# Optimization experiments

Hardware: AMD Instinct MI355X
Metric: run time of the kernel (lower is better)

The kernel has to match this reference:

```python
import jax, jax.numpy as jnp
import numpy as np
import math

N = 50000        # nodes
E = 800000       # edges (avg degree 16)
F_IN = 128
F_OUT = 64


def setup_inputs() -> dict:
    key = jax.random.key(0)
    k = jax.random.split(key, 7)
    stdv = 1.0 / math.sqrt(F_OUT)
    x = jax.random.normal(k[0], (N, F_IN), dtype=jnp.float32)
    t = jax.random.uniform(k[1], (N,), dtype=jnp.float32)
    src = jax.random.randint(k[2], (E,), 0, N, dtype=jnp.int64)
    dst = jax.random.randint(k[3], (E,), 0, N, dtype=jnp.int64)
    # sparse adjacency values (e.g. normalized adjacency weights)
    edge_vals = jax.random.uniform(k[4], (E,), dtype=jnp.float32)
    weight = jax.random.uniform(k[5], (F_IN, F_OUT), dtype=jnp.float32,
                                minval=-stdv, maxval=stdv)
    bias = jax.random.uniform(k[6], (F_OUT,), dtype=jnp.float32,
                              minval=-stdv, maxval=stdv)
    return {"x": x, "t": t, "src": src, "dst": dst,
            "edge_vals": edge_vals, "weight": weight, "bias": bias}


def reference(x, t, src, dst, edge_vals, weight, bias):
    # support = (X @ W) * t[:, None]   -- dense GEMM + per-row scale
    support = (x @ weight) * t[:, None]                 # [N, F_OUT]
    # spmm(adj, support): gather rows at src, scale by edge value, reduce by dst
    msgs = support[src] * edge_vals[:, None]            # [E, F_OUT]
    out = jax.ops.segment_sum(msgs, dst, num_segments=N)  # [N, F_OUT]
    return out + bias
```

## Files before the change

kernel.cpp:

```cpp
#include <hip/hip_runtime.h>
#include <hip/hip_bf16.h>

#define FIN 128
#define FOUT 64
#define TILE_ROWS 64

#define EPB 2048
#define NPB 32
#define NBUK_MAX 1600
#define CAP 768

#define OFF_HIST      6400000
#define OFF_BLOCKSUMS 8860000
#define OFF_TMP       8861024

#define SCAN_CHUNK 4096

typedef short bf16x8 __attribute__((ext_vector_type(8)));
typedef float f32x4  __attribute__((ext_vector_type(4)));

__device__ inline ushort f32_to_bf16_rne(float f) {
    unsigned u = __float_as_uint(f);
    u += 0x7FFFu + ((u >> 16) & 1u);
    return (ushort)(u >> 16);
}
__device__ inline float bf16_to_f32(ushort h) {
    return __uint_as_float((unsigned)h << 16);
}

union __align__(16) GemmHistSh {
    int    h[NBUK_MAX];
    ushort wt[FOUT * FIN];
};

__global__ __launch_bounds__(256) void gemm_hist_kernel(
    const float* __restrict__ x, const float* __restrict__ t,
    const float* __restrict__ W, ushort* __restrict__ support, int N,
    const int* __restrict__ dst, int* __restrict__ hist,
    int E, int SBP, int NBUK, int G, int GB)
{
    __shared__ GemmHistSh sh;
    const int tid = threadIdx.x;

    if (blockIdx.x >= GB) {
        const int hb    = blockIdx.x - GB;
        const int chunk = (hb & 7) * G + (hb >> 3);
        for (int i = tid; i < NBUK; i += 256) sh.h[i] = 0;
        __syncthreads();
        const int e0 = chunk * EPB;
        for (int i = tid; i < EPB; i += 256) {
            int e = e0 + i;
            if (e < E) atomicAdd(&sh.h[dst[e] >> 5], 1);
        }
        __syncthreads();
        for (int i = tid; i < NBUK; i += 256)
            hist[i * SBP + chunk] = sh.h[i];
        return;
    }

    const int lane = tid & 63;
    const int w    = tid >> 6;
    const int ln   = lane & 15;
    const int q    = lane >> 4;
    const int rowb = blockIdx.x * TILE_ROWS + w * 16;
    const int arow = rowb + ln;

    for (int idx = tid; idx < FIN * FOUT; idx += 256) {
        int k = idx >> 6;
        int n = idx & 63;
        sh.wt[n * FIN + (k ^ ((n & 7) << 3))] = f32_to_bf16_rne(W[idx]);
    }
    __syncthreads();

    f32x4 acc[4];
    #pragma unroll
    for (int nt = 0; nt < 4; ++nt)
        #pragma unroll
        for (int r = 0; r < 4; ++r) acc[nt][r] = 0.f;

    const bool aok = (arow < N);
    const float* xrow = &x[(size_t)arow * FIN];

    #pragma unroll
    for (int kc = 0; kc < 4; ++kc) {
        float xs[8];
        #pragma unroll
        for (int j = 0; j < 8; ++j) xs[j] = 0.f;
        if (aok) {
            float4 x0 = *(const float4*)&xrow[kc * 32 + q * 8];
            float4 x1 = *(const float4*)&xrow[kc * 32 + q * 8 + 4];
            xs[0] = x0.x; xs[1] = x0.y; xs[2] = x0.z; xs[3] = x0.w;
            xs[4] = x1.x; xs[5] = x1.y; xs[6] = x1.z; xs[7] = x1.w;
        }
        bf16x8 a;
        #pragma unroll
        for (int j = 0; j < 8; ++j) a[j] = (short)f32_to_bf16_rne(xs[j]);

        const int k0 = kc * 32 + q * 8;
        #pragma unroll
        for (int nt = 0; nt < 4; ++nt) {
            bf16x8 b = *(const bf16x8*)
                &sh.wt[(nt * 16 + ln) * FIN + (k0 ^ ((ln & 7) << 3))];
            acc[nt] = __builtin_amdgcn_mfma_f32_16x16x32_bf16(a, b, acc[nt], 0, 0, 0);
        }
    }

    #pragma unroll
    for (int reg = 0; reg < 4; ++reg) {
        int r = rowb + q * 4 + reg;
        if (r < N) {
            float tv = t[r];
            #pragma unroll
            for (int nt = 0; nt < 4; ++nt)
                support[(size_t)r * FOUT + nt * 16 + ln] =
                    f32_to_bf16_rne(acc[nt][reg] * tv);
        }
    }
}

__global__ __launch_bounds__(256) void scan_sums_kernel(
    const int* __restrict__ counts, int* __restrict__ blocksums, int M)
{
    __shared__ int red[256];
    const int tid  = threadIdx.x;
    const int base = blockIdx.x * SCAN_CHUNK + tid * 16;

    int s = 0;
    #pragma unroll
    for (int v = 0; v < 4; ++v) {
        int idx = base + v * 4;
        if (idx + 3 < M) {
            int4 c = *(const int4*)&counts[idx];
            s += c.x + c.y + c.z + c.w;
        } else {
            for (int i = 0; i < 4; ++i)
                if (idx + i < M) s += counts[idx + i];
        }
    }
    red[tid] = s;
    __syncthreads();
    #pragma unroll
    for (int d = 128; d > 0; d >>= 1) {
        if (tid < d) red[tid] += red[tid + d];
        __syncthreads();
    }
    if (tid == 0) blocksums[blockIdx.x] = red[0];
}

__global__ __launch_bounds__(256) void scan_apply_kernel(
    int* __restrict__ counts, const int* __restrict__ blocksums, int M, int NB)
{
    __shared__ int s[256];
    __shared__ int bex;
    const int tid  = threadIdx.x;
    const int base = blockIdx.x * SCAN_CHUNK + tid * 16;

    if (tid < 64) {
        int carry = 0;
        for (int w0 = 0; w0 < NB; w0 += 64) {
            int idx = w0 + tid;
            int v   = (idx < NB) ? blocksums[idx] : 0;
            int val = v;
            #pragma unroll
            for (int d = 1; d < 64; d <<= 1) {
                int n = __shfl_up(val, d);
                if (tid >= d) val += n;
            }
            if (idx == (int)blockIdx.x) bex = carry + val - v;
            carry += __shfl(val, 63);
        }
    }

    int c[16];
    int mysum = 0;
    #pragma unroll
    for (int v = 0; v < 4; ++v) {
        int idx = base + v * 4;
        int4 cc = make_int4(0, 0, 0, 0);
        if (idx + 3 < M) {
            cc = *(const int4*)&counts[idx];
        } else {
            if (idx + 0 < M) cc.x = counts[idx + 0];
            if (idx + 1 < M) cc.y = counts[idx + 1];
            if (idx + 2 < M) cc.z = counts[idx + 2];
            if (idx + 3 < M) cc.w = counts[idx + 3];
        }
        c[v * 4 + 0] = cc.x; c[v * 4 + 1] = cc.y;
        c[v * 4 + 2] = cc.z; c[v * 4 + 3] = cc.w;
        mysum += cc.x + cc.y + cc.z + cc.w;
    }
    s[tid] = mysum;
    __syncthreads();
    #pragma unroll
    for (int d = 1; d < 256; d <<= 1) {
        int add = (tid >= d) ? s[tid - d] : 0;
        __syncthreads();
        s[tid] += add;
        __syncthreads();
    }
    int ex = bex + s[tid] - mysum;
    #pragma unroll
    for (int i = 0; i < 16; ++i) {
        if (base + i < M) {
            counts[base + i] = ex;
            ex += c[i];
        }
    }
}

__global__ __launch_bounds__(256) void coarse_scatter_kernel(
    const int* __restrict__ src, const int* __restrict__ dst,
    const float* __restrict__ ev, const int* __restrict__ scanned,
    int2* __restrict__ tmp, int E, int SBP, int NBUK, int G)
{
    __shared__ int cur[NBUK_MAX];
    const int tid   = threadIdx.x;
    const int b     = blockIdx.x;
    const int chunk = (b & 7) * G + (b >> 3);
    for (int i = tid; i < NBUK; i += 256)
        cur[i] = scanned[i * SBP + chunk];
    __syncthreads();

    const int e0 = chunk * EPB;
    for (int i = tid; i < EPB; i += 256) {
        int e = e0 + i;
        if (e < E) {
            int d   = dst[e];
            int pos = atomicAdd(&cur[d >> 5], 1);
            tmp[pos] = make_int2(src[e] | ((d & (NPB - 1)) << 16),
                                 __float_as_int(ev[e]));
        }
    }
}

__global__ __launch_bounds__(256) void bucket_gather_kernel(
    const int* __restrict__ scanned, const int2* __restrict__ tmp,
    const ushort* __restrict__ support, const float* __restrict__ bias,
    float* __restrict__ out, int E, int N, int SBP, int NBUK)
{
    __shared__ int2 raw[CAP];
    __shared__ int2 sorted[CAP];
    __shared__ int  cnt[NPB];
    __shared__ int  starts[NPB + 1];
    __shared__ int  cur[NPB];

    const int tid   = threadIdx.x;
    const int w     = tid >> 6;
    const int lane  = tid & 63;
    const int B     = blockIdx.x;
    const int node0 = B * NPB;

    const int base   = scanned[B * SBP];
    const int endB   = (B + 1 < NBUK) ? scanned[(B + 1) * SBP] : E;
    const int nrec   = endB - base;
    const int placed = (nrec < CAP) ? nrec : CAP;

    if (tid < NPB) cnt[tid] = 0;
    __syncthreads();

    for (int i = tid; i < placed; i += 256) {
        int2 r = tmp[base + i];
        raw[i] = r;
        atomicAdd(&cnt[(r.x >> 16) & (NPB - 1)], 1);
    }
    __syncthreads();

    if (tid < 64) {
        int v   = (tid < NPB) ? cnt[tid] : 0;
        int val = v;
        #pragma unroll
        for (int d = 1; d < NPB; d <<= 1) {
            int n = __shfl_up(val, d);
            if (tid >= d) val += n;
        }
        if (tid < NPB) {
            starts[tid] = val - v;
            cur[tid]    = val - v;
        }
        if (tid == 0) starts[NPB] = placed;
    }
    __syncthreads();

    for (int i = tid; i < placed; i += 256) {
        int2 r  = raw[i];
        int pos = atomicAdd(&cur[(r.x >> 16) & (NPB - 1)], 1);
        sorted[pos] = r;
    }
    __syncthreads();

    const float bv = bias[lane];
    const int rbeg = starts[w * 8];
    const int rend = starts[w * 8 + 8];

    float accv = 0.f;
    int   curn = -1;

    int i = rbeg;
    while (i + 8 <= rend) {
        int2 r[8];
        #pragma unroll
        for (int u = 0; u < 8; ++u) r[u] = sorted[i + u];
        float v[8];
        #pragma unroll
        for (int u = 0; u < 8; ++u)
            v[u] = bf16_to_f32(support[(size_t)(r[u].x & 0xFFFF) * FOUT + lane]);
        #pragma unroll
        for (int u = 0; u < 8; ++u) {
            int n = (r[u].x >> 16) & (NPB - 1);
            if (n != curn) {
                if (curn >= 0 && node0 + curn < N)
                    out[(size_t)(node0 + curn) * FOUT + lane] = accv + bv;
                curn = n;
                accv = 0.f;
            }
            accv += v[u] * __int_as_float(r[u].y);
        }
        i += 8;
    }
    while (i < rend) {
        int2 a = sorted[i];
        float va = bf16_to_f32(support[(size_t)(a.x & 0xFFFF) * FOUT + lane]);
        int n = (a.x >> 16) & (NPB - 1);
        if (n != curn) {
            if (curn >= 0 && node0 + curn < N)
                out[(size_t)(node0 + curn) * FOUT + lane] = accv + bv;
            curn = n;
            accv = 0.f;
        }
        accv += va * __int_as_float(a.y);
        ++i;
    }
    if (curn >= 0 && node0 + curn < N)
        out[(size_t)(node0 + curn) * FOUT + lane] = accv + bv;

    for (int n = w; n < NPB; n += 4) {
        int node = node0 + n;
        if (node < N && cnt[n] == 0)
            out[(size_t)node * FOUT + lane] = bv;
    }

    if (nrec > CAP) {
        __threadfence();
        __syncthreads();
        for (int j = base + CAP + tid; j < endB; j += 256) {
            int2 r = tmp[j];
            int node = node0 + ((r.x >> 16) & (NPB - 1));
            float wgt = __int_as_float(r.y);
            for (int f = 0; f < FOUT; ++f) {
                float v = bf16_to_f32(support[(size_t)(r.x & 0xFFFF) * FOUT + f]);
                atomicAdd(&out[(size_t)node * FOUT + f], v * wgt);
            }
        }
    }
}

extern "C" void kernel_launch(void* const* d_in, const int* in_sizes, int n_in,
                              void* d_out, int out_size, void* d_ws, size_t ws_size,
                              hipStream_t stream) {
    const float* x    = (const float*)d_in[0];
    const float* t    = (const float*)d_in[1];
    const int*   src  = (const int*)d_in[2];
    const int*   dst  = (const int*)d_in[3];
    const float* ev   = (const float*)d_in[4];
    const float* W    = (const float*)d_in[5];
    const float* bias = (const float*)d_in[6];
    float* out = (float*)d_out;

    const int N = in_sizes[1];
    const int E = in_sizes[2];

    char*   ws        = (char*)d_ws;
    ushort* support   = (ushort*)ws;
    int*    hist      = (int*)(ws + OFF_HIST);
    int*    blocksums = (int*)(ws + OFF_BLOCKSUMS);
    int2*   tmp       = (int2*)(ws + OFF_TMP);

    const int GB   = (N + TILE_ROWS - 1) / TILE_ROWS;
    const int SBr  = (E + EPB - 1) / EPB;
    const int SBP  = ((SBr + 7) / 8) * 8;
    const int G    = SBP / 8;
    const int NBUK = (N + NPB - 1) / NPB;
    const int M    = NBUK * SBP;
    const int NBS  = (M + SCAN_CHUNK - 1) / SCAN_CHUNK;

    gemm_hist_kernel<<<GB + SBP, 256, 0, stream>>>(
        x, t, W, support, N, dst, hist, E, SBP, NBUK, G, GB);

    scan_sums_kernel<<<NBS, 256, 0, stream>>>(hist, blocksums, M);
    scan_apply_kernel<<<NBS, 256, 0, stream>>>(hist, blocksums, M, NBS);

    coarse_scatter_kernel<<<SBP, 256, 0, stream>>>(
        src, dst, ev, hist, tmp, E, SBP, NBUK, G);

    bucket_gather_kernel<<<NBUK, 256, 0, stream>>>(
        hist, tmp, support, bias, out, E, N, SBP, NBUK);
}
```

Before: 138.6 us.

## Replace per-chunk histogram scan with global bucket totals and atomic-claimed scatter

Drops the per-(bucket,chunk) histogram and its two scan kernels. Each histogram block now atomically adds into global bucket totals, and the last block to finish (tracked by a done counter) computes the exclusive scan. The scatter kernel stages edges in shared memory and claims contiguous ranges per bucket with one global atomic per bucket. Buckets grow to 64 nodes, which halves the bucket count and enlarges gather capacity. This removes two kernel launches and a large scan, at the cost of a memset, global atomics, and edge order within a bucket that is no longer deterministic.

After: 196.4 us. 1.42x slower.

```diff
diff --git a/kernel.cpp b/kernel.cpp
--- a/kernel.cpp
+++ b/kernel.cpp
@@ -6,15 +6,15 @@
 #define TILE_ROWS 64
 
 #define EPB 2048
-#define NPB 32
-#define NBUK_MAX 1600
-#define CAP 768
-
-#define OFF_HIST      6400000
-#define OFF_BLOCKSUMS 8860000
-#define OFF_TMP       8861024
-
-#define SCAN_CHUNK 4096
+#define NPB 64
+#define NBUK_MAX 800
+#define CAP 1408
+
+#define OFF_TOT   6400000
+#define OFF_DONE  6403200
+#define OFF_BASES 6403264
+#define OFF_CUR   6406464
+#define OFF_TMP   6409664
 
 typedef short bf16x8 __attribute__((ext_vector_type(8)));
 typedef float f32x4  __attribute__((ext_vector_type(4)));
@@ -36,25 +36,62 @@
 __global__ __launch_bounds__(256) void gemm_hist_kernel(
     const float* __restrict__ x, const float* __restrict__ t,
     const float* __restrict__ W, ushort* __restrict__ support, int N,
-    const int* __restrict__ dst, int* __restrict__ hist,
-    int E, int SBP, int NBUK, int G, int GB)
+    const int* __restrict__ dst, int* __restrict__ tot, int* __restrict__ done,
+    int* __restrict__ bases, int* __restrict__ cur,
+    int E, int SBP, int NBUK, int GB)
 {
     __shared__ GemmHistSh sh;
     const int tid = threadIdx.x;
 
     if (blockIdx.x >= GB) {
-        const int hb    = blockIdx.x - GB;
-        const int chunk = (hb & 7) * G + (hb >> 3);
+        __shared__ int amLast;
+        const int chunk = blockIdx.x - GB;
         for (int i = tid; i < NBUK; i += 256) sh.h[i] = 0;
         __syncthreads();
         const int e0 = chunk * EPB;
         for (int i = tid; i < EPB; i += 256) {
             int e = e0 + i;
-            if (e < E) atomicAdd(&sh.h[dst[e] >> 5], 1);
+            if (e < E) atomicAdd(&sh.h[dst[e] >> 6], 1);
         }
         __syncthreads();
         for (int i = tid; i < NBUK; i += 256)
-            hist[i * SBP + chunk] = sh.h[i];
+            if (sh.h[i]) atomicAdd(&tot[i], sh.h[i]);
+
+        __threadfence();
+        __syncthreads();
+        if (tid == 0)
+            amLast = (atomicAdd(done, 1) == SBP - 1);
+        __syncthreads();
+        if (!amLast) return;
+
+        __threadfence();
+        int v[4]; int s = 0;
+        #pragma unroll
+        for (int k = 0; k < 4; ++k) {
+            int j = tid * 4 + k;
+            v[k] = (j < NBUK)
+                 ? __hip_atomic_load(&tot[j], __ATOMIC_RELAXED,
+                                     __HIP_MEMORY_SCOPE_AGENT)
+                 : 0;
+            s += v[k];
+        }
+        __syncthreads();
+        sh.h[tid] = s;
+        __syncthreads();
+        #pragma unroll
+        for (int d = 1; d < 256; d <<= 1) {
+            int add = (tid >= d) ? sh.h[tid - d] : 0;
+            __syncthreads();
+            sh.h[tid] += add;
+            __syncthreads();
+        }
+        int ex = sh.h[tid] - s;
+        #pragma unroll
+        for (int k = 0; k < 4; ++k) {
+            int j = tid * 4 + k;
+            if (j < NBUK) { bases[j] = ex; cur[j] = ex; ex += v[k]; }
+        }
+        if (tid == 0) bases[NBUK] = E;
         return;
     }
 
@@ -118,125 +155,55 @@
     }
 }
 
-__global__ __launch_bounds__(256) void scan_sums_kernel(
-    const int* __restrict__ counts, int* __restrict__ blocksums, int M)
+__global__ __launch_bounds__(256) void scatter_kernel(
+    const int* __restrict__ src, const int* __restrict__ dst,
+    const float* __restrict__ ev, int* __restrict__ cur,
+    int2* __restrict__ tmp, int E, int NBUK)
 {
-    __shared__ int red[256];
-    const int tid  = threadIdx.x;
-    const int base = blockIdx.x * SCAN_CHUNK + tid * 16;
-
-    int s = 0;
-    #pragma unroll
-    for (int v = 0; v < 4; ++v) {
-        int idx = base + v * 4;
-        if (idx + 3 < M) {
-            int4 c = *(const int4*)&counts[idx];
-            s += c.x + c.y + c.z + c.w;
-        } else {
-            for (int i = 0; i < 4; ++i)
-                if (idx + i < M) s += counts[idx + i];
-        }
-    }
-    red[tid] = s;
-    __syncthreads();
-    #pragma unroll
-    for (int d = 128; d > 0; d >>= 1) {
-        if (tid < d) red[tid] += red[tid + d];
-        __syncthreads();
-    }
-    if (tid == 0) blocksums[blockIdx.x] = red[0];
-}
-
-__global__ __launch_bounds__(256) void scan_apply_kernel(
-    int* __restrict__ counts, const int* __restrict__ blocksums, int M, int NB)
-{
-    __shared__ int s[256];
-    __shared__ int bex;
-    const int tid  = threadIdx.x;
-    const int base = blockIdx.x * SCAN_CHUNK + tid * 16;
-
-    if (tid < 64) {
-        int carry = 0;
-        for (int w0 = 0; w0 < NB; w0 += 64) {
-            int idx = w0 + tid;
-            int v   = (idx < NB) ? blocksums[idx] : 0;
-            int val = v;
-            #pragma unroll
-            for (int d = 1; d < 64; d <<= 1) {
-                int n = __shfl_up(val, d);
-                if (tid >= d) val += n;
-            }
-            if (idx == (int)blockIdx.x) bex = carry + val - v;
-            carry += __shfl(val, 63);
-        }
-    }
-
-    int c[16];
-    int mysum = 0;
-    #pragma unroll
-    for (int v = 0; v < 4; ++v) {
-        int idx = base + v * 4;
-        int4 cc = make_int4(0, 0, 0, 0);
-        if (idx + 3 < M) {
-            cc = *(const int4*)&counts[idx];
-        } else {
-            if (idx + 0 < M) cc.x = counts[idx + 0];
-            if (idx + 1 < M) cc.y = counts[idx + 1];
-            if (idx + 2 < M) cc.z = counts[idx + 2];
-            if (idx + 3 < M) cc.w = counts[idx + 3];
-        }
-        c[v * 4 + 0] = cc.x; c[v * 4 + 1] = cc.y;
-        c[v * 4 + 2] = cc.z; c[v * 4 + 3] = cc.w;
-        mysum += cc.x + cc.y + cc.z + cc.w;
-    }
-    s[tid] = mysum;
-    __syncthreads();
-    #pragma unroll
-    for (int d = 1; d < 256; d <<= 1) {
-        int add = (tid >= d) ? s[tid - d] : 0;
-        __syncthreads();
-        s[tid] += add;
-        __syncthreads();
-    }
-    int ex = bex + s[tid] - mysum;
-    #pragma unroll
-    for (int i = 0; i < 16; ++i) {
-        if (base + i < M) {
-            counts[base + i] = ex;
-            ex += c[i];
-        }
-    }
-}
-
-__global__ __launch_bounds__(256) void coarse_scatter_kernel(
-    const int* __restrict__ src, const int* __restrict__ dst,
-    const float* __restrict__ ev, const int* __restrict__ scanned,
-    int2* __restrict__ tmp, int E, int SBP, int NBUK, int G)
-{
-    __shared__ int cur[NBUK_MAX];
-    const int tid   = threadIdx.x;
-    const int b     = blockIdx.x;
-    const int chunk = (b & 7) * G + (b >> 3);
-    for (int i = tid; i < NBUK; i += 256)
-        cur[i] = scanned[i * SBP + chunk];
-    __syncthreads();
-
-    const int e0 = chunk * EPB;
+    __shared__ int2   stage[EPB];
+    __shared__ ushort bkt[EPB];
+    __shared__ int    h[NBUK_MAX];
+    __shared__ int    c[NBUK_MAX];
+
+    const int tid = threadIdx.x;
+    const int e0  = blockIdx.x * EPB;
+
+    for (int i = tid; i < NBUK; i += 256) h[i] = 0;
+    __syncthreads();
+
     for (int i = tid; i < EPB; i += 256) {
         int e = e0 + i;
         if (e < E) {
-            int d   = dst[e];
-            int pos = atomicAdd(&cur[d >> 5], 1);
-            tmp[pos] = make_int2(src[e] | ((d & (NPB - 1)) << 16),
+            int d = dst[e];
+            int j = d >> 6;
+            stage[i] = make_int2(src[e] | ((d & (NPB - 1)) << 16),
                                  __float_as_int(ev[e]));
+            bkt[i] = (ushort)j;
+            atomicAdd(&h[j], 1);
+        } else {
+            bkt[i] = 0xFFFF;
+        }
+    }
+    __syncthreads();
+
+    for (int j = tid; j < NBUK; j += 256) {
+        int hj = h[j];
+        if (hj) c[j] = atomicAdd(&cur[j], hj);
+    }
+    __syncthreads();
+
+    for (int i = tid; i < EPB; i += 256) {
+        if (bkt[i] != 0xFFFF) {
+            int pos = atomicAdd(&c[bkt[i]], 1);
+            tmp[pos] = stage[i];
         }
     }
 }
 
 __global__ __launch_bounds__(256) void bucket_gather_kernel(
-    const int* __restrict__ scanned, const int2* __restrict__ tmp,
+    const int* __restrict__ bases, const int2* __restrict__ tmp,
     const ushort* __restrict__ support, const float* __restrict__ bias,
-    float* __restrict__ out, int E, int N, int SBP, int NBUK)
+    float* __restrict__ out, int E, int N, int NBUK)
 {
     __shared__ int2 raw[CAP];
     __shared__ int2 sorted[CAP];
@@ -250,8 +217,8 @@
     const int B     = blockIdx.x;
     const int node0 = B * NPB;
 
-    const int base   = scanned[B * SBP];
-    const int endB   = (B + 1 < NBUK) ? scanned[(B + 1) * SBP] : E;
+    const int base   = bases[B];
+    const int endB   = bases[B + 1];
     const int nrec   = endB - base;
     const int placed = (nrec < CAP) ? nrec : CAP;
 
@@ -266,17 +233,15 @@
     __syncthreads();
 
     if (tid < 64) {
-        int v   = (tid < NPB) ? cnt[tid] : 0;
+        int v   = cnt[tid];
         int val = v;
         #pragma unroll
         for (int d = 1; d < NPB; d <<= 1) {
             int n = __shfl_up(val, d);
             if (tid >= d) val += n;
         }
-        if (tid < NPB) {
-            starts[tid] = val - v;
-            cur[tid]    = val - v;
-        }
+        starts[tid] = val - v;
+        cur[tid]    = val - v;
         if (tid == 0) starts[NPB] = placed;
     }
     __syncthreads();
@@ -289,8 +254,8 @@
     __syncthreads();
 
     const float bv = bias[lane];
-    const int rbeg = starts[w * 8];
-    const int rend = starts[w * 8 + 8];
+    const int rbeg = starts[w * 16];
+    const int rend = starts[w * 16 + 16];
 
     float accv = 0.f;
     int   curn = -1;
@@ -369,29 +334,25 @@
     const int N = in_sizes[1];
     const int E = in_sizes[2];
 
-    char*   ws        = (char*)d_ws;
-    ushort* support   = (ushort*)ws;
-    int*    hist      = (int*)(ws + OFF_HIST);
-    int*    blocksums = (int*)(ws + OFF_BLOCKSUMS);
-    int2*   tmp       = (int2*)(ws + OFF_TMP);
+    char*   ws      = (char*)d_ws;
+    ushort* support = (ushort*)ws;
+    int*    tot     = (int*)(ws + OFF_TOT);
+    int*    done    = (int*)(ws + OFF_DONE);
+    int*    bases   = (int*)(ws + OFF_BASES);
+    int*    cur     = (int*)(ws + OFF_CUR);
+    int2*   tmp     = (int2*)(ws + OFF_TMP);
 
     const int GB   = (N + TILE_ROWS - 1) / TILE_ROWS;
-    const int SBr  = (E + EPB - 1) / EPB;
-    const int SBP  = ((SBr + 7) / 8) * 8;
-    const int G    = SBP / 8;
+    const int SBP  = (E + EPB - 1) / EPB;
     const int NBUK = (N + NPB - 1) / NPB;
-    const int M    = NBUK * SBP;
-    const int NBS  = (M + SCAN_CHUNK - 1) / SCAN_CHUNK;
+
+    hipMemsetAsync(ws + OFF_TOT, 0, OFF_BASES - OFF_TOT, stream);
 
     gemm_hist_kernel<<<GB + SBP, 256, 0, stream>>>(
-        x, t, W, support, N, dst, hist, E, SBP, NBUK, G, GB);
-
-    scan_sums_kernel<<<NBS, 256, 0, stream>>>(hist, blocksums, M);
-    scan_apply_kernel<<<NBS, 256, 0, stream>>>(hist, blocksums, M, NBS);
-
-    coarse_scatter_kernel<<<SBP, 256, 0, stream>>>(
-        src, dst, ev, hist, tmp, E, SBP, NBUK, G);
+        x, t, W, support, N, dst, tot, done, bases, cur, E, SBP, NBUK, GB);
+
+    scatter_kernel<<<SBP, 256, 0, stream>>>(src, dst, ev, cur, tmp, E, NBUK);
 
     bucket_gather_kernel<<<NBUK, 256, 0, stream>>>(
-        hist, tmp, support, bias, out, E, N, SBP, NBUK);
-}
+        bases, tmp, support, bias, out, E, N, NBUK);
+}
```
